# Optimization experiments

Hardware: AMD Instinct MI355X
Metric: run time of the kernel (lower is better)

The kernel has to match this reference:

```python
import jax, jax.numpy as jnp
import numpy as np

K_NN = 8        # neighbors
RADIUS = 0.1    # neighbor distance cutoff


def setup_inputs() -> dict:
    key = jax.random.key(0)
    k1, k2 = jax.random.split(key)
    B, N, KS = 2, 8192, 16  # batch, points, mask slots
    pc = jax.random.uniform(k1, (B, N, 3), dtype=jnp.float32)
    mask = jax.random.uniform(k2, (B, N, KS), dtype=jnp.float32)
    return {"pc": pc, "mask": mask}


def _knn(k, pc):
    # squared pairwise distances via gemm: (B,N,N)
    sq = jnp.sum(pc * pc, axis=-1)
    d2 = sq[:, :, None] + sq[:, None, :] - 2.0 * jnp.einsum("bnd,bmd->bnm", pc, pc)
    d2 = jnp.maximum(d2, 0.0)
    neg_d2, idx = jax.lax.top_k(-d2, k)          # k smallest distances
    dist = jnp.sqrt(jnp.maximum(-neg_d2, 0.0))   # (B,N,k) euclidean
    return dist, idx


def reference(pc, mask):
    # mask: (B,N,KS) -> (B,KS,N)
    mask_t = jnp.transpose(mask, (0, 2, 1))
    dist, idx = _knn(K_NN, pc)                   # (B,N,k) each
    # replace out-of-radius neighbors with the self index (nearest = self)
    self_idx = idx[:, :, :1]                     # (B,N,1)
    idx = jnp.where(dist > RADIUS, self_idx, idx)
    idx = jax.lax.stop_gradient(idx)
    # grouping_operation: (B,KS,N) gathered at (B,N,k) -> (B,KS,N,k)
    nn_mask = jax.vmap(lambda f, i: f[:, i])(mask_t, idx)
    # loss_norm=1: L1 norm over mask-slot dim (dim=1), mean over k, mean overall
    diff = mask_t[:, :, :, None] - nn_mask       # (B,KS,N,k)
    loss = jnp.sum(jnp.abs(diff), axis=1).mean(axis=-1)  # (B,N)
    return loss.mean()
```

## Files before the change

kernel.cpp:

```cpp
#include <hip/hip_runtime.h>

#define BATCH 2
#define NPTS  8192
#define KS    16
#define KNN   8
#define R2LOOSE 0.0101f
#define KEYMASK 0xFFFFE000u
#define NCELL   1000
#define CSTRIDE 1024

#define QB       64
#define NWAVE    8
#define NTHREADS 512
#define CAP      32
#define TILEC    1024
#define NBLK     (BATCH * NPTS / QB)

__device__ __forceinline__ int cell_of(float x, float y, float z) {
    int cx = (int)(x * 10.0f); cx = cx > 9 ? 9 : cx;
    int cy = (int)(y * 10.0f); cy = cy > 9 ? 9 : cy;
    int cz = (int)(z * 10.0f); cz = cz > 9 ? 9 : cz;
    return (cx * 10 + cy) * 10 + cz;
}

__global__ void count_kernel(const float* __restrict__ pc, int* cfill) {
    const int i = blockIdx.x * 1024 + threadIdx.x;
    const float x = pc[3 * i], y = pc[3 * i + 1], z = pc[3 * i + 2];
    const int b = i >> 13;
    atomicAdd(&cfill[b * CSTRIDE + cell_of(x, y, z)], 1);
}

__global__ __launch_bounds__(1024) void scan_kernel(int* cfill, int* cstart,
                                                    float* out) {
    __shared__ int arr[1024];
    const int b = blockIdx.x, t = threadIdx.x;
    if (b == 0 && t == 0) out[0] = 0.0f;
    const int cnt = cfill[b * CSTRIDE + t];
    arr[t] = cnt;
    __syncthreads();
    for (int off = 1; off < 1024; off <<= 1) {
        const int v = (t >= off) ? arr[t - off] : 0;
        __syncthreads();
        arr[t] += v;
        __syncthreads();
    }
    const int excl = arr[t] - cnt;
    cstart[b * CSTRIDE + t] = excl;
    cfill[b * CSTRIDE + t]  = excl;
}

__global__ void scatter_kernel(const float* __restrict__ pc,
                               float4* __restrict__ cs,
                               int* __restrict__ sidx, int* cfill) {
    const int i = blockIdx.x * 1024 + threadIdx.x;
    const float x = pc[3 * i], y = pc[3 * i + 1], z = pc[3 * i + 2];
    const int b = i >> 13;
    const float sq = fmaf(z, z, fmaf(y, y, x * x));
    const int pos = atomicAdd(&cfill[b * CSTRIDE + cell_of(x, y, z)], 1);
    cs[b * NPTS + pos]   = make_float4(x, y, z, -0.5f * sq);
    sidx[b * NPTS + pos] = i & (NPTS - 1);
}

__global__ __launch_bounds__(512) void knn_loss_kernel(
    const float4* __restrict__ cs,
    const int*    __restrict__ sidx,
    const int*    __restrict__ cstart,
    const float*  __restrict__ mask,
    float* __restrict__ out)
{
    __shared__ float4   tile[TILEC];
    __shared__ int      tsp[TILEC];
    __shared__ unsigned sbuf[CAP * NTHREADS];
    __shared__ int      fidx[QB * KNN];
    __shared__ int      qid[QB];
    __shared__ float    red[NWAVE];

    const int t = threadIdx.x;
    const int q = t & (QB - 1);
    const int s = t >> 6;
    const int su = __builtin_amdgcn_readfirstlane(s);
    const int blk = blockIdx.x;
    const int b  = blk >> 7;
    const int q0 = (blk & 127) * QB;
    const int qpos = q0 + q;

    const float4* csb = cs + b * NPTS;
    const float4 qc = csb[qpos];
    const int    qi = sidx[b * NPTS + qpos];
    if (s == 0) qid[q] = qi;

    const float qx = qc.x, qy = qc.y, qz = qc.z;
    const float qs = -2.0f * qc.w;
    const float negthr = (qs - R2LOOSE) * 0.5f;
    const unsigned SENT = (__float_as_uint(R2LOOSE) & KEYMASK) | 0x1FFFu;

    int lex = cell_of(qx, qy, qz);
    int cmn = lex, cmx = lex;
#pragma unroll
    for (int off = 32; off; off >>= 1) {
        cmn = min(cmn, __shfl_xor(cmn, off));
        cmx = max(cmx, __shfl_xor(cmx, off));
    }
    const int cfirst = __builtin_amdgcn_readfirstlane(cmn);
    const int clast  = __builtin_amdgcn_readfirstlane(cmx);

    int lo0 = cfirst - 111, h0 = clast - 89;
    int lo1 = cfirst - 11,  h1 = clast + 11;
    int lo2 = cfirst + 89,  h2 = clast + 111;
    lo0 = min(max(lo0, 0), 1000);
    lo1 = min(max(lo1, 0), 1000);
    lo2 = min(max(lo2, 0), 1000);
    int hp0 = min(max(h0 + 1, 0), 1000);
    int hp1 = min(max(h1 + 1, 0), 1000);
    int hp2 = min(max(h2 + 1, 0), 1000);
    lo1 = max(lo1, hp0);
    lo2 = max(lo2, hp1);

    const int* csp = cstart + b * CSTRIDE;
    const int P0 = csp[lo0], E0 = csp[hp0];
    const int P1 = csp[lo1], E1 = csp[hp1];
    const int P2 = csp[lo2], E2 = csp[hp2];
    const int L0 = max(0, E0 - P0);
    const int L1 = max(0, E1 - P1);
    const int L2 = max(0, E2 - P2);
    const int C  = L0 + L1 + L2;

    int cnt = 0;
    auto EVAL = [&](const float4& c, int spos) {
        const float tt = fmaf(c.x, qx, fmaf(c.y, qy, fmaf(c.z, qz, c.w)));
        const float d2 = fmaxf(fmaf(-2.0f, tt, qs), 0.0f);
        const unsigned key =
            (__float_as_uint(d2) & KEYMASK) | (unsigned)spos;
        const int slot = cnt < (CAP - 1) ? cnt : (CAP - 1);
        sbuf[slot * NTHREADS + t] = key;
        cnt += (tt >= negthr) ? 1 : 0;
    };

    for (int tb = 0; tb < C; tb += TILEC) {
        const int nt = min(TILEC, C - tb);
        for (int p = t; p < nt; p += NTHREADS) {
            const int g = tb + p;
            int sp = P0 + g;
            sp = (g >= L0)      ? (P1 + (g - L0))      : sp;
            sp = (g >= L0 + L1) ? (P2 + (g - L0 - L1)) : sp;
            tile[p] = csb[sp];
            tsp[p]  = sp;
        }
        __syncthreads();

        int j = (su * nt) >> 3;
        const int e = ((su + 1) * nt) >> 3;
        for (; j + 4 <= e; j += 4) {
            const float4 c0 = tile[j],     c1 = tile[j + 1];
            const float4 c2 = tile[j + 2], c3 = tile[j + 3];
            const int s0 = tsp[j],     s1 = tsp[j + 1];
            const int s2 = tsp[j + 2], s3 = tsp[j + 3];
            EVAL(c0, s0); EVAL(c1, s1); EVAL(c2, s2); EVAL(c3, s3);
        }
        for (; j < e; ++j) { const float4 c0 = tile[j]; EVAL(c0, tsp[j]); }
        __syncthreads();
    }

    unsigned md[KNN];
#pragma unroll
    for (int k = 0; k < KNN; ++k) md[k] = SENT;
    const int m = cnt < CAP ? cnt : CAP;
    for (int k = 0; k < m; ++k) {
        unsigned ky = sbuf[k * NTHREADS + t];
#pragma unroll
        for (int i = 0; i < KNN; ++i) {
            const unsigned mn = min(ky, md[i]);
            const unsigned mx = max(ky, md[i]);
            md[i] = mn; ky = mx;
        }
    }
    __syncthreads();

    {
        uint4* bp = (uint4*)&sbuf[t * KNN];
        bp[0] = make_uint4(md[0], md[1], md[2], md[3]);
        bp[1] = make_uint4(md[4], md[5], md[6], md[7]);
    }
    __syncthreads();

    if (s == 0) {
        for (int l = 1; l < NWAVE; ++l) {
            const uint4* lp = (const uint4*)&sbuf[(l * QB + q) * KNN];
            const uint4 r0 = lp[0], r1 = lp[1];
            const unsigned tk[8] = {r0.x, r0.y, r0.z, r0.w,
                                    r1.x, r1.y, r1.z, r1.w};
#pragma unroll
            for (int k = 0; k < 8; ++k) {
                unsigned ky = tk[k];
                if (ky < md[KNN - 1]) {
#pragma unroll
                    for (int i = 0; i < KNN; ++i) {
                        const unsigned mn = min(ky, md[i]);
                        const unsigned mx = max(ky, md[i]);
                        md[i] = mn; ky = mx;
                    }
                }
            }
        }
#pragma unroll
        for (int k = 0; k < KNN; ++k) {
            const unsigned ky = md[k];
            int nb;
            if (ky >= SENT) {
                nb = qi;
            } else {
                const int sp = (int)(ky & 0x1FFFu);
                const float4 cc = csb[sp];
                const float dx = cc.x - qx;
                const float dy = cc.y - qy;
                const float dz = cc.z - qz;
                const float d2 = fmaf(dx, dx, fmaf(dy, dy, dz * dz));
                nb = (sqrtf(d2) > 0.1f) ? qi : sidx[b * NPTS + sp];
            }
            fidx[q * KNN + k] = nb;
        }
    }
    __syncthreads();

    const int q2 = t >> 3;
    const int j2 = t & 7;
    const int qg = qid[q2];
    const int nb = fidx[q2 * KNN + j2];
    const float* mrow = mask + ((size_t)b * NPTS + qg) * KS;
    const float* nrow = mask + ((size_t)b * NPTS + nb) * KS;
    float acc = 0.0f;
#pragma unroll
    for (int c = 0; c < KS; c += 4) {
        const float4 a = *(const float4*)(mrow + c);
        const float4 v = *(const float4*)(nrow + c);
        acc += fabsf(a.x - v.x) + fabsf(a.y - v.y) +
               fabsf(a.z - v.z) + fabsf(a.w - v.w);
    }

#pragma unroll
    for (int off = 32; off > 0; off >>= 1) acc += __shfl_down(acc, off);
    if ((t & 63) == 0) red[s] = acc;
    __syncthreads();
    if (t == 0) {
        float sum = 0.0f;
#pragma unroll
        for (int i = 0; i < NWAVE; ++i) sum += red[i];
        atomicAdd(out, sum * (1.0f / (BATCH * NPTS * KNN)));
    }
}

extern "C" void kernel_launch(void* const* d_in, const int* in_sizes, int n_in,
                              void* d_out, int out_size, void* d_ws, size_t ws_size,
                              hipStream_t stream) {
    const float* pc   = (const float*)d_in[0];
    const float* mask = (const float*)d_in[1];
    float* out = (float*)d_out;

    float4* cs     = (float4*)d_ws;
    int*    sidx   = (int*)((char*)d_ws + 262144);
    int*    cstart = (int*)((char*)d_ws + 327680);
    int*    cfill  = (int*)((char*)d_ws + 335872);

    hipMemsetAsync(cfill, 0, 2 * CSTRIDE * sizeof(int), stream);
    hipLaunchKernelGGL(count_kernel,   dim3(16), dim3(1024), 0, stream, pc, cfill);
    hipLaunchKernelGGL(scan_kernel,    dim3(2),  dim3(1024), 0, stream,
                       cfill, cstart, out);
    hipLaunchKernelGGL(scatter_kernel, dim3(16), dim3(1024), 0, stream,
                       pc, cs, sidx, cfill);
    hipLaunchKernelGGL(knn_loss_kernel, dim3(NBLK), dim3(512), 0, stream,
                       cs, sidx, cstart, mask, out);
}
```

Before: 84.03 us.

## Replace memset+count+scan+scatter with per-block histograms and fused scan-scatter

Counting now builds a per-block shared-memory histogram written to a 16x1024 buffer, which removes the memset and the global atomics. Each scatter block then sums the 8 block histograms of its batch, runs the prefix scan itself, adds the counts of earlier blocks as its offset, and scatters using shared-memory atomics. This cuts the preprocessing from a memset plus three launches to two launches. The cost is that the scan is repeated in all 16 blocks, and the order of points within a cell changes, which could affect tie-breaking.

```diff
diff --git a/kernel.cpp b/kernel.cpp
--- a/kernel.cpp
+++ b/kernel.cpp
@@ -23,20 +23,36 @@
     return (cx * 10 + cy) * 10 + cz;
 }
 
-__global__ void count_kernel(const float* __restrict__ pc, int* cfill) {
-    const int i = blockIdx.x * 1024 + threadIdx.x;
+__global__ __launch_bounds__(1024) void count_kernel(
+    const float* __restrict__ pc, int* __restrict__ hist16) {
+    __shared__ int h[1024];
+    const int blk = blockIdx.x, t = threadIdx.x;
+    h[t] = 0;
+    __syncthreads();
+    const int i = blk * 1024 + t;
     const float x = pc[3 * i], y = pc[3 * i + 1], z = pc[3 * i + 2];
-    const int b = i >> 13;
-    atomicAdd(&cfill[b * CSTRIDE + cell_of(x, y, z)], 1);
-}
-
-__global__ __launch_bounds__(1024) void scan_kernel(int* cfill, int* cstart,
-                                                    float* out) {
+    atomicAdd(&h[cell_of(x, y, z)], 1);
+    __syncthreads();
+    hist16[blk * 1024 + t] = h[t];
+}
+
+__global__ __launch_bounds__(1024) void scatter_kernel(
+    const float* __restrict__ pc, const int* __restrict__ hist16,
+    float4* __restrict__ cs, int* __restrict__ sidx,
+    int* __restrict__ cstart, float* __restrict__ out) {
     __shared__ int arr[1024];
-    const int b = blockIdx.x, t = threadIdx.x;
-    if (b == 0 && t == 0) out[0] = 0.0f;
-    const int cnt = cfill[b * CSTRIDE + t];
-    arr[t] = cnt;
+    const int blk = blockIdx.x, t = threadIdx.x;
+    const int b  = blk >> 3;
+    const int j0 = b * 8;
+
+    int sum = 0, bel = 0;
+#pragma unroll
+    for (int j = 0; j < 8; ++j) {
+        const int v = hist16[(j0 + j) * 1024 + t];
+        sum += v;
+        bel += ((j0 + j) < blk) ? v : 0;
+    }
+    arr[t] = sum;
     __syncthreads();
     for (int off = 1; off < 1024; off <<= 1) {
         const int v = (t >= off) ? arr[t - off] : 0;
@@ -44,19 +60,17 @@
         arr[t] += v;
         __syncthreads();
     }
-    const int excl = arr[t] - cnt;
-    cstart[b * CSTRIDE + t] = excl;
-    cfill[b * CSTRIDE + t]  = excl;
-}
-
-__global__ void scatter_kernel(const float* __restrict__ pc,
-                               float4* __restrict__ cs,
-                               int* __restrict__ sidx, int* cfill) {
-    const int i = blockIdx.x * 1024 + threadIdx.x;
+    const int excl = arr[t] - sum;
+    if ((blk & 7) == 0) cstart[b * CSTRIDE + t] = excl;
+    if (blk == 0 && t == 0) out[0] = 0.0f;
+    __syncthreads();
+    arr[t] = excl + bel;
+    __syncthreads();
+
+    const int i = blk * 1024 + t;
     const float x = pc[3 * i], y = pc[3 * i + 1], z = pc[3 * i + 2];
-    const int b = i >> 13;
     const float sq = fmaf(z, z, fmaf(y, y, x * x));
-    const int pos = atomicAdd(&cfill[b * CSTRIDE + cell_of(x, y, z)], 1);
+    const int pos = atomicAdd(&arr[cell_of(x, y, z)], 1);
     cs[b * NPTS + pos]   = make_float4(x, y, z, -0.5f * sq);
     sidx[b * NPTS + pos] = i & (NPTS - 1);
 }
@@ -259,14 +273,12 @@
     float4* cs     = (float4*)d_ws;
     int*    sidx   = (int*)((char*)d_ws + 262144);
     int*    cstart = (int*)((char*)d_ws + 327680);
-    int*    cfill  = (int*)((char*)d_ws + 335872);
-
-    hipMemsetAsync(cfill, 0, 2 * CSTRIDE * sizeof(int), stream);
-    hipLaunchKernelGGL(count_kernel,   dim3(16), dim3(1024), 0, stream, pc, cfill);
-    hipLaunchKernelGGL(scan_kernel,    dim3(2),  dim3(1024), 0, stream,
-                       cfill, cstart, out);
+    int*    hist16 = (int*)((char*)d_ws + 335872);
+
+    hipLaunchKernelGGL(count_kernel,   dim3(16), dim3(1024), 0, stream,
+                       pc, hist16);
     hipLaunchKernelGGL(scatter_kernel, dim3(16), dim3(1024), 0, stream,
-                       pc, cs, sidx, cfill);
+                       pc, hist16, cs, sidx, cstart, out);
     hipLaunchKernelGGL(knn_loss_kernel, dim3(NBLK), dim3(512), 0, stream,
                        cs, sidx, cstart, mask, out);
 }
```

Result: faster. 79.81 us (-5.0%).
